# Optimization experiments

Hardware: AMD Instinct MI355X
Metric: run time of the kernel (lower is better)

## Reference

```python
import jax, jax.numpy as jnp
import numpy as np

B, S, D = 4, 2048, 512
H, DK, DV = 8, 64, 64


def setup_inputs() -> dict:
    key = jax.random.key(0)
    ks = jax.random.split(key, 9)
    inp = {
        "input_Q": jax.random.normal(ks[0], (B, S, D), dtype=jnp.float32),
        "input_K": jax.random.normal(ks[1], (B, S, D), dtype=jnp.float32),
        "input_V": jax.random.normal(ks[2], (B, S, D), dtype=jnp.float32),
        "attn_mask": jax.random.bernoulli(ks[3], 0.1, (B, S, S)),
        "other": jax.random.normal(ks[4], (B, S, S), dtype=jnp.float32),
        # nn.Linear weights stored [out_features, in_features]
        "W_Q": jax.random.normal(ks[5], (H * DK, D), dtype=jnp.float32) * (1.0 / np.sqrt(D)),
        "W_K": jax.random.normal(ks[6], (H * DK, D), dtype=jnp.float32) * (1.0 / np.sqrt(D)),
        "W_V": jax.random.normal(ks[7], (H * DV, D), dtype=jnp.float32) * (1.0 / np.sqrt(D)),
        "W_fc": jax.random.normal(ks[8], (D, H * DV), dtype=jnp.float32) * (1.0 / np.sqrt(H * DV)),
    }
    return inp


def reference(input_Q, input_K, input_V, attn_mask, other, W_Q, W_K, W_V, W_fc):
    b, s, _ = input_Q.shape
    # projections: y = x @ W.T, then split heads -> [B,H,S,dk]
    Q = (input_Q @ W_Q.T).reshape(b, s, H, DK).transpose(0, 2, 1, 3)
    K = (input_K @ W_K.T).reshape(b, s, H, DK).transpose(0, 2, 1, 3)
    V = (input_V @ W_V.T).reshape(b, s, H, DV).transpose(0, 2, 1, 3)
    scale = 1.0 / np.sqrt(DK).astype(np.float32)
    scores = jnp.einsum("bhqd,bhkd->bhqk", Q, K) * scale  # [B,H,S,S]
    scores = scores + other[:, None, :, :]  # additive bias broadcast over heads
    scores = jnp.where(attn_mask[:, None, :, :], jnp.float32(-1e9), scores)
    attn = jax.nn.softmax(scores, axis=-1)
    context = jnp.einsum("bhqk,bhkd->bhqd", attn, V)  # [B,H,S,DV]
    context = context.transpose(0, 2, 1, 3).reshape(b, s, H * DV)
    output = context @ W_fc.T  # dropout is identity at inference
    return (output, attn)
```

## Files before the change

### kernel.cpp

```cpp
#include <hip/hip_runtime.h>

#define BB 4
#define SS 2048
#define DDIM 512
#define HH 8
#define MTOK (BB*SS)
#define BHN (BB*HH)

typedef _Float16 f16;
typedef __attribute__((ext_vector_type(8))) _Float16 half8;
typedef __attribute__((ext_vector_type(4))) _Float16 half4;
typedef __attribute__((ext_vector_type(4))) float float4v;
typedef __attribute__((ext_vector_type(4))) int int4v;

#define SCALE_L2E 0.180336880073616f
#define L2E 1.44269504088896f
#define EBIAS 4.0f
#define MASKVAL -65504.0f

__device__ __forceinline__ float4v mfma_k32(half8 a, half8 b, float4v c) {
  return __builtin_amdgcn_mfma_f32_16x16x32_f16(a, b, c, 0, 0, 0);
}

__device__ __forceinline__ half8 cvt8(float4v a, float4v b) {
  half8 r;
  r[0] = (f16)a[0]; r[1] = (f16)a[1]; r[2] = (f16)a[2]; r[3] = (f16)a[3];
  r[4] = (f16)b[0]; r[5] = (f16)b[1]; r[6] = (f16)b[2]; r[7] = (f16)b[3];
  return r;
}

__global__ __launch_bounds__(256) void detect_mask_kernel(
    const unsigned int* __restrict__ m, unsigned int* __restrict__ flag) {
  unsigned int v = 0;
  const int base = blockIdx.x * 1024;
  for (int j = threadIdx.x; j < 1024; j += 256)
    if (m[base + j] > 1u) v = 1u;
  if (v) atomicOr(flag, 1u);
}

__global__ __launch_bounds__(256) void gemm_qkv(
    const float* __restrict__ inQ, const float* __restrict__ inK,
    const float* __restrict__ inV, const float* __restrict__ WQ,
    const float* __restrict__ WK, const float* __restrict__ WV,
    f16* __restrict__ Qp, f16* __restrict__ Kfrag, f16* __restrict__ Vfrag) {
  __shared__ f16 As[128][40];
  __shared__ f16 Bs[128][40];
  const int z = blockIdx.z;
  const float* A = (z == 0) ? inQ : (z == 1) ? inK : inV;
  const float* W = (z == 0) ? WQ : (z == 1) ? WK : WV;
  const int t = threadIdx.x;
  const int bm = blockIdx.x * 128;
  const int bn = blockIdx.y * 128;
  const int w = t >> 6, ln = t & 63;
  const int wr = w >> 1, wc = w & 1;
  const int lr = ln & 15, lg = ln >> 4;
  const int srow = t >> 1, scol = (t & 1) * 16;

  float4v acc[4][4] = {};

  for (int k0 = 0; k0 < 512; k0 += 32) {
    {
      const float* ap = A + (size_t)(bm + srow) * 512 + k0 + scol;
      float4v x0 = *(const float4v*)ap,       x1 = *(const float4v*)(ap + 4);
      float4v x2 = *(const float4v*)(ap + 8), x3 = *(const float4v*)(ap + 12);
      *(half8*)&As[srow][scol]     = cvt8(x0, x1);
      *(half8*)&As[srow][scol + 8] = cvt8(x2, x3);
    }
    {
      const float* wp = W + (size_t)(bn + srow) * 512 + k0 + scol;
      float4v x0 = *(const float4v*)wp,       x1 = *(const float4v*)(wp + 4);
      float4v x2 = *(const float4v*)(wp + 8), x3 = *(const float4v*)(wp + 12);
      *(half8*)&Bs[srow][scol]     = cvt8(x0, x1);
      *(half8*)&Bs[srow][scol + 8] = cvt8(x2, x3);
    }
    __syncthreads();
    half8 af[4], bf[4];
    #pragma unroll
    for (int m = 0; m < 4; m++) af[m] = *(const half8*)&As[wr * 64 + m * 16 + lr][lg * 8];
    #pragma unroll
    for (int n = 0; n < 4; n++) bf[n] = *(const half8*)&Bs[wc * 64 + n * 16 + lr][lg * 8];
    #pragma unroll
    for (int m = 0; m < 4; m++)
      #pragma unroll
      for (int n = 0; n < 4; n++) acc[m][n] = mfma_k32(af[m], bf[n], acc[m][n]);
    __syncthreads();
  }

  #pragma unroll
  for (int m = 0; m < 4; m++) {
    int row = bm + wr * 64 + m * 16 + lg * 4;
    #pragma unroll
    for (int n = 0; n < 4; n++) {
      int col = bn + wc * 64 + n * 16 + lr;
      int b_ = row >> 11, s_ = row & 2047, h_ = col >> 6, d_ = col & 63;
      if (z == 0) {
        #pragma unroll
        for (int r = 0; r < 4; r++)
          Qp[(size_t)(row + r) * 512 + col] = (f16)acc[m][n][r];
      } else if (z == 1) {
        #pragma unroll
        for (int r = 0; r < 4; r++) {
          int tok = s_ + r;
          Kfrag[((((size_t)(b_ * 8 + h_)) * 128 + (tok >> 4)) * 2 + (d_ >> 5)) * 512 +
                ((tok & 15) + 16 * ((d_ >> 3) & 3)) * 8 + (d_ & 7)] =
              (f16)acc[m][n][r];
        }
      } else {
        half4 ph;
        ph[0] = (f16)acc[m][n][0]; ph[1] = (f16)acc[m][n][1];
        ph[2] = (f16)acc[m][n][2]; ph[3] = (f16)acc[m][n][3];
        *(half4*)&Vfrag[((((size_t)(b_ * 8 + h_)) * 64 + (s_ >> 5)) * 4 + (d_ >> 4)) * 512 +
                        ((d_ & 15) + 16 * ((s_ >> 2) & 3)) * 8 + ((s_ >> 2) & 4)] = ph;
      }
    }
  }
}

__global__ __launch_bounds__(256) void gemm_out(const f16* __restrict__ ctx,
                                                const float* __restrict__ W,
                                                float* __restrict__ Out) {
  __shared__ f16 As[128][40];
  __shared__ f16 Bs[128][40];
  const int t = threadIdx.x;
  const int bm = blockIdx.x * 128;
  const int bn = blockIdx.y * 128;
  const int w = t >> 6, ln = t & 63;
  const int wr = w >> 1, wc = w & 1;
  const int lr = ln & 15, lg = ln >> 4;
  const int srow = t >> 1, scol = (t & 1) * 16;

  float4v acc[4][4] = {};

  for (int k0 = 0; k0 < 512; k0 += 32) {
    {
      const f16* ap = ctx + (size_t)(bm + srow) * 512 + k0 + scol;
      *(half8*)&As[srow][scol]     = *(const half8*)(ap);
      *(half8*)&As[srow][scol + 8] = *(const half8*)(ap + 8);
    }
    {
      const float* wp = W + (size_t)(bn + srow) * 512 + k0 + scol;
      float4v x0 = *(const float4v*)wp,       x1 = *(const float4v*)(wp + 4);
      float4v x2 = *(const float4v*)(wp + 8), x3 = *(const float4v*)(wp + 12);
      *(half8*)&Bs[srow][scol]     = cvt8(x0, x1);
      *(half8*)&Bs[srow][scol + 8] = cvt8(x2, x3);
    }
    __syncthreads();
    half8 af[4], bf[4];
    #pragma unroll
    for (int m = 0; m < 4; m++) af[m] = *(const half8*)&As[wr * 64 + m * 16 + lr][lg * 8];
    #pragma unroll
    for (int n = 0; n < 4; n++) bf[n] = *(const half8*)&Bs[wc * 64 + n * 16 + lr][lg * 8];
    #pragma unroll
    for (int m = 0; m < 4; m++)
      #pragma unroll
      for (int n = 0; n < 4; n++) acc[m][n] = mfma_k32(af[m], bf[n], acc[m][n]);
    __syncthreads();
  }

  #pragma unroll
  for (int m = 0; m < 4; m++) {
    int row = bm + wr * 64 + m * 16 + lg * 4;
    #pragma unroll
    for (int n = 0; n < 4; n++) {
      int col = bn + wc * 64 + n * 16 + lr;
      #pragma unroll
      for (int r = 0; r < 4; r++)
        Out[(size_t)(row + r) * 512 + col] = acc[m][n][r];
    }
  }
}

#define LOADK(dst, st) {                                        \
    const f16* p_ = kfb + (size_t)(st) * 2048;                  \
    dst##0 = *(const half8*)(p_);                               \
    dst##1 = *(const half8*)(p_ + 512);                         \
    dst##2 = *(const half8*)(p_ + 1024);                        \
    dst##3 = *(const half8*)(p_ + 1536); }
#define LOADV(dst, st) {                                        \
    const f16* p_ = vfb + (size_t)(st) * 2048;                  \
    dst##0 = *(const half8*)(p_);                               \
    dst##1 = *(const half8*)(p_ + 512);                         \
    dst##2 = *(const half8*)(p_ + 1024);                        \
    dst##3 = *(const half8*)(p_ + 1536); }

__global__ __launch_bounds__(512, 2) void attn_fused(
    const f16* __restrict__ Qp, const f16* __restrict__ Kfrag,
    const f16* __restrict__ Vfrag, const float* __restrict__ other,
    const unsigned char* __restrict__ mask8, const int* __restrict__ mask32,
    const unsigned int* __restrict__ flag, float* __restrict__ attn_out,
    f16* __restrict__ ctx) {
  __shared__ f16 othm[16][2056];

  const int t = threadIdx.x;
  const int bid = blockIdx.x;
  const int b = bid & 3;
  const int qblk = (bid >> 2) * 16;
  const int w = t >> 6, ln = t & 63;
  const int lr = ln & 15, lg = ln >> 4;
  const bool use8 = (*flag) != 0;

  {
    const int q = t >> 5, k0 = (t & 31) * 64;
    const size_t base = ((size_t)b * SS + qblk + q) * SS + k0;
    const float* op = other + base;
    if (use8) {
      const unsigned char* mp = mask8 + base;
      #pragma unroll
      for (int g = 0; g < 8; g++) {
        unsigned int mw0 = *(const unsigned int*)(mp + g * 8);
        unsigned int mw1 = *(const unsigned int*)(mp + g * 8 + 4);
        float4v o0 = *(const float4v*)(op + g * 8);
        float4v o1 = *(const float4v*)(op + g * 8 + 4);
        float4v r0, r1;
        #pragma unroll
        for (int r = 0; r < 4; r++) {
          r0[r] = ((mw0 >> (8 * r)) & 0xffu) ? MASKVAL : fmaf(o0[r], L2E, -EBIAS);
          r1[r] = ((mw1 >> (8 * r)) & 0xffu) ? MASKVAL : fmaf(o1[r], L2E, -EBIAS);
        }
        *(half8*)&othm[q][k0 + g * 8] = cvt8(r0, r1);
      }
    } else {
      const int* mp = mask32 + base;
      #pragma unroll
      for (int g = 0; g < 8; g++) {
        int4v m0 = *(const int4v*)(mp + g * 8);
        int4v m1 = *(const int4v*)(mp + g * 8 + 4);
        float4v o0 = *(const float4v*)(op + g * 8);
        float4v o1 = *(const float4v*)(op + g * 8 + 4);
        float4v r0, r1;
        #pragma unroll
        for (int r = 0; r < 4; r++) {
          r0[r] = m0[r] ? MASKVAL : fmaf(o0[r], L2E, -EBIAS);
          r1[r] = m1[r] ? MASKVAL : fmaf(o1[r], L2E, -EBIAS);
        }
        *(half8*)&othm[q][k0 + g * 8] = cvt8(r0, r1);
      }
    }
  }
  __syncthreads();

  const int h = w, bh = b * 8 + h;
  const f16* qp = Qp + ((size_t)b * SS + qblk + lr) * 512 + h * 64 + lg * 8;
  const half8 qf0 = *(const half8*)qp;
  const half8 qf1 = *(const half8*)(qp + 32);

  const f16* kfb = Kfrag + (size_t)bh * 128 * 2 * 512 + ln * 8;
  const f16* vfb = Vfrag + (size_t)bh * 64 * 4 * 512 + ln * 8;
  float* abase = attn_out + ((size_t)bh * SS + qblk + lr) * SS;

  half8 kA0, kA1, kA2, kA3, kB0, kB1, kB2, kB3;
  half8 vA0, vA1, vA2, vA3, vB0, vB1, vB2, vB3;

  float rs = 0.f;
  LOADK(kA, 0);

  #define BODYA(kf, st) {                                                 \
    float4v s0 = {}, s1 = {};                                             \
    s0 = mfma_k32(kf##0, qf0, s0);                                        \
    s0 = mfma_k32(kf##1, qf1, s0);                                        \
    s1 = mfma_k32(kf##2, qf0, s1);                                        \
    s1 = mfma_k32(kf##3, qf1, s1);                                        \
    const int kl = (st) * 32;                                             \
    const half4 o40 = *(const half4*)&othm[lr][kl + lg * 4];              \
    const half4 o41 = *(const half4*)&othm[lr][kl + 16 + lg * 4];         \
    float4v ev0, ev1;                                                     \
    _Pragma("unroll")                                                     \
    for (int r = 0; r < 4; r++) {                                         \
      ev0[r] = exp2f(fmaf(s0[r], SCALE_L2E, (float)o40[r]));              \
      ev1[r] = exp2f(fmaf(s1[r], SCALE_L2E, (float)o41[r]));              \
    }                                                                     \
    rs += (ev0[0] + ev0[1]) + (ev0[2] + ev0[3]) +                         \
          (ev1[0] + ev1[1]) + (ev1[2] + ev1[3]);                          \
  }

  for (int st2 = 0; st2 < 32; st2++) {
    const int se = st2 * 2;
    {
      LOADK(kB, se + 1);
      BODYA(kA, se);
    }
    {
      const int so = se + 1;
      const int stn = (so < 63) ? so + 1 : 63;
      LOADK(kA, stn);
      BODYA(kB, so);
    }
  }
  #undef BODYA

  rs += __shfl_xor(rs, 16);
  rs += __shfl_xor(rs, 32);
  const float invl = 1.0f / rs;

  float4v cacc0 = {}, cacc1 = {}, cacc2 = {}, cacc3 = {};
  LOADK(kA, 0);
  LOADV(vA, 0);

  #define BODYB(kf, vf, st) {                                             \
    float4v s0 = {}, s1 = {};                                             \
    s0 = mfma_k32(kf##0, qf0, s0);                                        \
    s0 = mfma_k32(kf##1, qf1, s0);                                        \
    s1 = mfma_k32(kf##2, qf0, s1);                                        \
    s1 = mfma_k32(kf##3, qf1, s1);                                        \
    const int kl = (st) * 32;                                             \
    const half4 o40 = *(const half4*)&othm[lr][kl + lg * 4];              \
    const half4 o41 = *(const half4*)&othm[lr][kl + 16 + lg * 4];         \
    float4v ev0, ev1;                                                     \
    _Pragma("unroll")                                                     \
    for (int r = 0; r < 4; r++) {                                         \
      ev0[r] = exp2f(fmaf(s0[r], SCALE_L2E, (float)o40[r]));              \
      ev1[r] = exp2f(fmaf(s1[r], SCALE_L2E, (float)o41[r]));              \
    }                                                                     \
    float4v av0 = ev0 * invl, av1 = ev1 * invl;                           \
    *(float4v*)(abase + kl + lg * 4) = av0;                               \
    *(float4v*)(abase + kl + 16 + lg * 4) = av1;                          \
    half8 pa8 = cvt8(av0, av1);                                           \
    cacc0 = mfma_k32(pa8, vf##0, cacc0);                                  \
    cacc1 = mfma_k32(pa8, vf##1, cacc1);                                  \
    cacc2 = mfma_k32(pa8, vf##2, cacc2);                                  \
    cacc3 = mfma_k32(pa8, vf##3, cacc3);                                  \
  }

  for (int st2 = 0; st2 < 32; st2++) {
    const int se = st2 * 2;
    {
      LOADK(kB, se + 1);
      LOADV(vB, se + 1);
      BODYB(kA, vA, se);
    }
    {
      const int so = se + 1;
      const int stn = (so < 63) ? so + 1 : 63;
      LOADK(kA, stn);
      LOADV(vA, stn);
      BODYB(kB, vB, so);
    }
  }
  #undef BODYB

  #pragma unroll
  for (int r = 0; r < 4; r++) {
    const size_t crow = ((size_t)b * SS + qblk + lg * 4 + r) * 512 + h * 64;
    ctx[crow + 0 * 16 + lr] = (f16)cacc0[r];
    ctx[crow + 1 * 16 + lr] = (f16)cacc1[r];
    ctx[crow + 2 * 16 + lr] = (f16)cacc2[r];
    ctx[crow + 3 * 16 + lr] = (f16)cacc3[r];
  }
}

extern "C" void kernel_launch(void* const* d_in, const int* in_sizes, int n_in,
                              void* d_out, int out_size, void* d_ws, size_t ws_size,
                              hipStream_t stream) {
  const float* inQ   = (const float*)d_in[0];
  const float* inK   = (const float*)d_in[1];
  const float* inV   = (const float*)d_in[2];
  const void*  mask  = d_in[3];
  const float* other = (const float*)d_in[4];
  const float* WQ    = (const float*)d_in[5];
  const float* WK    = (const float*)d_in[6];
  const float* WV    = (const float*)d_in[7];
  const float* WF    = (const float*)d_in[8];

  char* ws = (char*)d_ws;
  size_t off = 0;
  unsigned int* flag = (unsigned int*)(ws + off); off += 256;
  f16* Qp    = (f16*)(ws + off); off += (size_t)MTOK * 512 * 2;
  f16* Kfrag = (f16*)(ws + off); off += (size_t)MTOK * 512 * 2;
  f16* Vfrag = (f16*)(ws + off); off += (size_t)MTOK * 512 * 2;
  f16* ctx   = (f16*)(ws + off); off += (size_t)MTOK * 512 * 2;
  if (ws_size < off) return;

  float* outp  = (float*)d_out;
  float* attnp = outp + (size_t)MTOK * DDIM;

  hipMemsetAsync(flag, 0, 256, stream);
  detect_mask_kernel<<<64, 256, 0, stream>>>((const unsigned int*)mask, flag);

  gemm_qkv<<<dim3(64, 4, 3), 256, 0, stream>>>(inQ, inK, inV, WQ, WK, WV,
                                               Qp, Kfrag, Vfrag);

  attn_fused<<<512, 512, 0, stream>>>(
      Qp, Kfrag, Vfrag, other, (const unsigned char*)mask, (const int*)mask,
      flag, attnp, ctx);

  gemm_out<<<dim3(64, 4), 256, 0, stream>>>(ctx, WF, outp);
}
```

Before: 364.0 us.

## Split attention key dimension across 16 waves and loop heads inside block

The attention kernel now launches 1024 threads, and each of 16 waves owns a 128-key slice instead of a whole head. Each block loops over all 8 heads. Instead of a two-pass recompute, scores are exponentiated once, kept as fp16 registers, and fed to the PV MFMA unnormalized. Row sums and partial context accumulators are reduced across waves through shared memory, and the attention probabilities are then normalized and stored. This removes the second QK pass but adds two block-wide barriers per head, a large shared-memory reduction buffer, and lower occupancy per CU. Stored attention weights are also rounded to fp16 before normalization.

```diff
diff --git a/kernel.cpp b/kernel.cpp
--- a/kernel.cpp
+++ b/kernel.cpp
@@ -170,26 +170,22 @@
   }
 }
 
-#define LOADK(dst, st) {                                        \
-    const f16* p_ = kfb + (size_t)(st) * 2048;                  \
+#define LOADT(dst, base, st) {                                  \
+    const f16* p_ = (base) + (size_t)(st) * 2048;               \
     dst##0 = *(const half8*)(p_);                               \
     dst##1 = *(const half8*)(p_ + 512);                         \
     dst##2 = *(const half8*)(p_ + 1024);                        \
     dst##3 = *(const half8*)(p_ + 1536); }
-#define LOADV(dst, st) {                                        \
-    const f16* p_ = vfb + (size_t)(st) * 2048;                  \
-    dst##0 = *(const half8*)(p_);                               \
-    dst##1 = *(const half8*)(p_ + 512);                         \
-    dst##2 = *(const half8*)(p_ + 1024);                        \
-    dst##3 = *(const half8*)(p_ + 1536); }
-
-__global__ __launch_bounds__(512, 2) void attn_fused(
+
+__global__ __launch_bounds__(1024) void attn_fused(
     const f16* __restrict__ Qp, const f16* __restrict__ Kfrag,
     const f16* __restrict__ Vfrag, const float* __restrict__ other,
     const unsigned char* __restrict__ mask8, const int* __restrict__ mask32,
     const unsigned int* __restrict__ flag, float* __restrict__ attn_out,
     f16* __restrict__ ctx) {
   __shared__ f16 othm[16][2056];
+  __shared__ float red[16][16];
+  __shared__ float red2[16][16][66];
 
   const int t = threadIdx.x;
   const int bid = blockIdx.x;
@@ -200,13 +196,13 @@
   const bool use8 = (*flag) != 0;
 
   {
-    const int q = t >> 5, k0 = (t & 31) * 64;
+    const int q = t >> 6, k0 = (t & 63) * 32;
     const size_t base = ((size_t)b * SS + qblk + q) * SS + k0;
     const float* op = other + base;
     if (use8) {
       const unsigned char* mp = mask8 + base;
       #pragma unroll
-      for (int g = 0; g < 8; g++) {
+      for (int g = 0; g < 4; g++) {
         unsigned int mw0 = *(const unsigned int*)(mp + g * 8);
         unsigned int mw1 = *(const unsigned int*)(mp + g * 8 + 4);
         float4v o0 = *(const float4v*)(op + g * 8);
@@ -222,7 +218,7 @@
     } else {
       const int* mp = mask32 + base;
       #pragma unroll
-      for (int g = 0; g < 8; g++) {
+      for (int g = 0; g < 4; g++) {
         int4v m0 = *(const int4v*)(mp + g * 8);
         int4v m1 = *(const int4v*)(mp + g * 8 + 4);
         float4v o0 = *(const float4v*)(op + g * 8);
@@ -239,30 +235,28 @@
   }
   __syncthreads();
 
-  const int h = w, bh = b * 8 + h;
-  const f16* qp = Qp + ((size_t)b * SS + qblk + lr) * 512 + h * 64 + lg * 8;
-  const half8 qf0 = *(const half8*)qp;
-  const half8 qf1 = *(const half8*)(qp + 32);
-
-  const f16* kfb = Kfrag + (size_t)bh * 128 * 2 * 512 + ln * 8;
-  const f16* vfb = Vfrag + (size_t)bh * 64 * 4 * 512 + ln * 8;
-  float* abase = attn_out + ((size_t)bh * SS + qblk + lr) * SS;
+  const int q_g = qblk + lr;
+  const f16* kfb = Kfrag + (size_t)(b * 8) * 131072 + ln * 8;
+  const f16* vfb = Vfrag + (size_t)(b * 8) * 131072 + ln * 8;
+  const f16* qpp = Qp + ((size_t)b * SS + q_g) * 512 + lg * 8;
+
+  half8 qf0 = *(const half8*)(qpp);
+  half8 qf1 = *(const half8*)(qpp + 32);
 
   half8 kA0, kA1, kA2, kA3, kB0, kB1, kB2, kB3;
-  half8 vA0, vA1, vA2, vA3, vB0, vB1, vB2, vB3;
-
-  float rs = 0.f;
-  LOADK(kA, 0);
-
-  #define BODYA(kf, st) {                                                 \
+  half8 vf0, vf1, vf2, vf3;
+
+  LOADT(kA, kfb, w * 4 + 0);
+
+  #define BODY(kf, edst, g) {                                             \
     float4v s0 = {}, s1 = {};                                             \
     s0 = mfma_k32(kf##0, qf0, s0);                                        \
     s0 = mfma_k32(kf##1, qf1, s0);                                        \
     s1 = mfma_k32(kf##2, qf0, s1);                                        \
     s1 = mfma_k32(kf##3, qf1, s1);                                        \
-    const int kl = (st) * 32;                                             \
-    const half4 o40 = *(const half4*)&othm[lr][kl + lg * 4];              \
-    const half4 o41 = *(const half4*)&othm[lr][kl + 16 + lg * 4];         \
+    const int kbase = w * 128 + (g) * 32;                                 \
+    const half4 o40 = *(const half4*)&othm[lr][kbase + lg * 4];           \
+    const half4 o41 = *(const half4*)&othm[lr][kbase + 16 + lg * 4];      \
     float4v ev0, ev1;                                                     \
     _Pragma("unroll")                                                     \
     for (int r = 0; r < 4; r++) {                                         \
@@ -271,81 +265,92 @@
     }                                                                     \
     rs += (ev0[0] + ev0[1]) + (ev0[2] + ev0[3]) +                         \
           (ev1[0] + ev1[1]) + (ev1[2] + ev1[3]);                          \
-  }
-
-  for (int st2 = 0; st2 < 32; st2++) {
-    const int se = st2 * 2;
-    {
-      LOADK(kB, se + 1);
-      BODYA(kA, se);
-    }
-    {
-      const int so = se + 1;
-      const int stn = (so < 63) ? so + 1 : 63;
-      LOADK(kA, stn);
-      BODYA(kB, so);
-    }
-  }
-  #undef BODYA
-
-  rs += __shfl_xor(rs, 16);
-  rs += __shfl_xor(rs, 32);
-  const float invl = 1.0f / rs;
-
-  float4v cacc0 = {}, cacc1 = {}, cacc2 = {}, cacc3 = {};
-  LOADK(kA, 0);
-  LOADV(vA, 0);
-
-  #define BODYB(kf, vf, st) {                                             \
-    float4v s0 = {}, s1 = {};                                             \
-    s0 = mfma_k32(kf##0, qf0, s0);                                        \
-    s0 = mfma_k32(kf##1, qf1, s0);                                        \
-    s1 = mfma_k32(kf##2, qf0, s1);                                        \
-    s1 = mfma_k32(kf##3, qf1, s1);                                        \
-    const int kl = (st) * 32;                                             \
-    const half4 o40 = *(const half4*)&othm[lr][kl + lg * 4];              \
-    const half4 o41 = *(const half4*)&othm[lr][kl + 16 + lg * 4];         \
-    float4v ev0, ev1;                                                     \
-    _Pragma("unroll")                                                     \
-    for (int r = 0; r < 4; r++) {                                         \
-      ev0[r] = exp2f(fmaf(s0[r], SCALE_L2E, (float)o40[r]));              \
-      ev1[r] = exp2f(fmaf(s1[r], SCALE_L2E, (float)o41[r]));              \
-    }                                                                     \
-    float4v av0 = ev0 * invl, av1 = ev1 * invl;                           \
-    *(float4v*)(abase + kl + lg * 4) = av0;                               \
-    *(float4v*)(abase + kl + 16 + lg * 4) = av1;                          \
-    half8 pa8 = cvt8(av0, av1);                                           \
-    cacc0 = mfma_k32(pa8, vf##0, cacc0);                                  \
-    cacc1 = mfma_k32(pa8, vf##1, cacc1);                                  \
-    cacc2 = mfma_k32(pa8, vf##2, cacc2);                                  \
-    cacc3 = mfma_k32(pa8, vf##3, cacc3);                                  \
-  }
-
-  for (int st2 = 0; st2 < 32; st2++) {
-    const int se = st2 * 2;
-    {
-      LOADK(kB, se + 1);
-      LOADV(vB, se + 1);
-      BODYB(kA, vA, se);
-    }
-    {
-      const int so = se + 1;
-      const int stn = (so < 63) ? so + 1 : 63;
-      LOADK(kA, stn);
-      LOADV(vA, stn);
-      BODYB(kB, vB, so);
-    }
-  }
-  #undef BODYB
-
-  #pragma unroll
-  for (int r = 0; r < 4; r++) {
-    const size_t crow = ((size_t)b * SS + qblk + lg * 4 + r) * 512 + h * 64;
-    ctx[crow + 0 * 16 + lr] = (f16)cacc0[r];
-    ctx[crow + 1 * 16 + lr] = (f16)cacc1[r];
-    ctx[crow + 2 * 16 + lr] = (f16)cacc2[r];
-    ctx[crow + 3 * 16 + lr] = (f16)cacc3[r];
-  }
+    edst = cvt8(ev0, ev1);                                                \
+    cacc0 = mfma_k32(edst, vf0, cacc0);                                   \
+    cacc1 = mfma_k32(edst, vf1, cacc1);                                   \
+    cacc2 = mfma_k32(edst, vf2, cacc2);                                   \
+    cacc3 = mfma_k32(edst, vf3, cacc3);                                   \
+  }
+
+  #define ASTORE(e, g) {                                                  \
+    float4v av0, av1;                                                     \
+    av0[0] = (float)e[0] * invl; av0[1] = (float)e[1] * invl;             \
+    av0[2] = (float)e[2] * invl; av0[3] = (float)e[3] * invl;             \
+    av1[0] = (float)e[4] * invl; av1[1] = (float)e[5] * invl;             \
+    av1[2] = (float)e[6] * invl; av1[3] = (float)e[7] * invl;             \
+    *(float4v*)(abase + (g) * 32 + lg * 4) = av0;                         \
+    *(float4v*)(abase + (g) * 32 + 16 + lg * 4) = av1;                    \
+  }
+
+  for (int h = 0; h < 8; ++h) {
+    const int bh = b * 8 + h;
+    const f16* kfb_nx = (h < 7) ? kfb + 131072 : kfb;
+
+    float rs = 0.f;
+    float4v cacc0 = {}, cacc1 = {}, cacc2 = {}, cacc3 = {};
+    half8 e0, e1, e2, e3;
+
+    LOADT(vf, vfb, w * 4 + 0);
+    LOADT(kB, kfb, w * 4 + 1);
+    BODY(kA, e0, 0);
+
+    LOADT(vf, vfb, w * 4 + 1);
+    LOADT(kA, kfb, w * 4 + 2);
+    BODY(kB, e1, 1);
+
+    LOADT(vf, vfb, w * 4 + 2);
+    LOADT(kB, kfb, w * 4 + 3);
+    BODY(kA, e2, 2);
+
+    LOADT(vf, vfb, w * 4 + 3);
+    LOADT(kA, kfb_nx, w * 4 + 0);
+    BODY(kB, e3, 3);
+
+    const int hn = (h < 7) ? h + 1 : 7;
+    half8 qn0 = *(const half8*)(qpp + hn * 64);
+    half8 qn1 = *(const half8*)(qpp + hn * 64 + 32);
+
+    rs += __shfl_xor(rs, 16);
+    rs += __shfl_xor(rs, 32);
+    if (ln < 16) red[w][lr] = rs;
+    #pragma unroll
+    for (int r = 0; r < 4; r++) {
+      red2[w][lg * 4 + r][0 * 16 + lr] = cacc0[r];
+      red2[w][lg * 4 + r][1 * 16 + lr] = cacc1[r];
+      red2[w][lg * 4 + r][2 * 16 + lr] = cacc2[r];
+      red2[w][lg * 4 + r][3 * 16 + lr] = cacc3[r];
+    }
+    __syncthreads();
+
+    float lsum = 0.f;
+    #pragma unroll
+    for (int ww = 0; ww < 16; ww++) lsum += red[ww][lr];
+    const float invl = 1.0f / lsum;
+
+    float* abase = attn_out + ((size_t)bh * SS + q_g) * SS + w * 128;
+    ASTORE(e0, 0);
+    ASTORE(e1, 1);
+    ASTORE(e2, 2);
+    ASTORE(e3, 3);
+
+    {
+      float s16 = 0.f, l2 = 0.f;
+      #pragma unroll
+      for (int ww = 0; ww < 16; ww++) {
+        s16 += red2[ww][w][ln];
+        l2 += red[ww][w];
+      }
+      ctx[((size_t)b * SS + qblk + w) * 512 + h * 64 + ln] = (f16)(s16 / l2);
+    }
+    __syncthreads();
+
+    qf0 = qn0;
+    qf1 = qn1;
+    kfb = kfb_nx;
+    vfb = (h < 7) ? vfb + 131072 : vfb;
+  }
+  #undef BODY
+  #undef ASTORE
 }
 
 extern "C" void kernel_launch(void* const* d_in, const int* in_sizes, int n_in,
@@ -379,7 +384,7 @@
   gemm_qkv<<<dim3(64, 4, 3), 256, 0, stream>>>(inQ, inK, inV, WQ, WK, WV,
                                                Qp, Kfrag, Vfrag);
 
-  attn_fused<<<512, 512, 0, stream>>>(
+  attn_fused<<<512, 1024, 0, stream>>>(
       Qp, Kfrag, Vfrag, other, (const unsigned char*)mask, (const int*)mask,
       flag, attnp, ctx);
 
```

Measured after the change: 334.1 us. 1.09x faster.
